# Optimization experiments

Hardware: AMD Instinct MI355X
Metric: run time of the kernel (lower is better)

Reference implementation:

```python
import jax, jax.numpy as jnp
import numpy as np

EPS = 1e-06        # normalize eps and log eps (module's self.eps)
PDIST_EPS = 1e-06  # torch.nn.PairwiseDistance default eps: ||x1 - x2 + eps||_2

A, C, F = 4096, 8, 64


def setup_inputs() -> dict:
    key = jax.random.key(0)
    x = jax.random.normal(key, (A, C, F), dtype=jnp.float32)
    return {"x": x}


def reference(x) -> jnp.ndarray:
    a = x.shape[0]
    c = x.shape[1]
    # F.normalize(p=2, dim=-1, eps=EPS): x / max(||x||_2, eps)
    nrm = jnp.linalg.norm(x, axis=-1, keepdims=True)
    xn = x / jnp.maximum(nrm, EPS)
    # pairwise cosine similarity per group: [C, A, A]
    sim = jnp.einsum('acf,bcf->cab', xn, xn)
    # mask self-similarity on the diagonal with -1
    diag = jnp.eye(a, dtype=bool)[None, :, :]
    sim = jnp.where(diag, -1.0, sim)
    # nearest neighbor per (c, a): argmax over b -> [C, A] -> [A, C]
    idx = jnp.argmax(sim, axis=-1).T
    # gather matched embeddings: x_match[a, c, f] = xn[idx[a, c], c, f]
    x_match = xn[idx, jnp.arange(c)[None, :], :]
    # PairwiseDistance(p=2, eps=1e-6): ||x - x_match + eps||_2 over last dim
    min_dist = jnp.linalg.norm(xn - x_match + PDIST_EPS, axis=-1)
    loss = -jnp.mean(jnp.log(min_dist + EPS))
    return loss
```

## Files before the change

### kernel.cpp

```cpp
#include <hip/hip_runtime.h>
#include <math.h>

#define AN 4096
#define CN 8
#define FN 64
#define ACN (AN*CN)

typedef __attribute__((ext_vector_type(8))) short bf16x8;
typedef __attribute__((ext_vector_type(4))) float f32x4;

__device__ inline unsigned short f2bf(float f) {
    unsigned u = __float_as_uint(f);
    unsigned r = ((u >> 16) & 1) + 0x7FFFu;
    return (unsigned short)((u + r) >> 16);
}

__global__ __launch_bounds__(256) void k1_normalize(const float* __restrict__ x,
                                                    unsigned short* __restrict__ xnb,
                                                    float* __restrict__ inv)
{
    int tid  = threadIdx.x;
    int grp  = tid >> 4;
    int slot = tid & 15;
    #pragma unroll
    for (int s = 0; s < 4; ++s) {
        int V = blockIdx.x * 64 + s * 16 + grp;
        const float4 v = *(const float4*)(x + (size_t)V * FN + slot * 4);
        float ss = v.x*v.x + v.y*v.y + v.z*v.z + v.w*v.w;
        ss += __shfl_xor(ss, 1);
        ss += __shfl_xor(ss, 2);
        ss += __shfl_xor(ss, 4);
        ss += __shfl_xor(ss, 8);
        float sc = 1.0f / fmaxf(sqrtf(ss), 1e-6f);
        int a = V >> 3, c = V & 7;
        ushort4 ob;
        ob.x = f2bf(v.x * sc); ob.y = f2bf(v.y * sc);
        ob.z = f2bf(v.z * sc); ob.w = f2bf(v.w * sc);
        *(ushort4*)(xnb + ((size_t)c * AN + a) * FN + slot * 4) = ob;
        if (slot == 0) inv[V] = sc;
    }
}

__global__ __launch_bounds__(256, 2) void k2_argmax(const unsigned short* __restrict__ xnb,
                                                    unsigned int* __restrict__ pP)
{
    __shared__ uint4 lds4[3 * 1024];

    int blk  = blockIdx.x;
    int half = blk & 1;
    int rt   = (blk >> 1) & 31;
    int c    = blk >> 6;
    int a0   = rt * 128;
    int b0base = half * 2048;

    const uint4* __restrict__ Xc4 = (const uint4*)(xnb + (size_t)c * AN * FN);

    int tid  = threadIdx.x;
    int lane = tid & 63;
    int w    = tid >> 6;
    int wr   = w >> 1;
    int wc   = w & 1;
    int l15  = lane & 15;
    int quad = lane >> 4;

    int srow   = tid >> 3;
    int schunk = tid & 7;

    #pragma unroll
    for (int s = 0; s < 4; ++s) {
        int r = srow + 32 * s;
        lds4[r * 8 + (schunk ^ (r & 7))] = Xc4[(size_t)(a0 + r) * 8 + schunk];
    }
    #pragma unroll
    for (int s = 0; s < 4; ++s) {
        int r = srow + 32 * s;
        lds4[1024 + r * 8 + (schunk ^ (r & 7))] = Xc4[(size_t)(b0base + r) * 8 + schunk];
    }
    __syncthreads();

    bf16x8 afr[4][2];
    #pragma unroll
    for (int mi = 0; mi < 4; ++mi)
        #pragma unroll
        for (int ks = 0; ks < 2; ++ks) {
            int r  = wr * 64 + mi * 16 + l15;
            int ch = (ks * 4 + quad) ^ (r & 7);
            afr[mi][ks] = ((const bf16x8*)lds4)[r * 8 + ch];
        }

    float bestp[16];
    #pragma unroll
    for (int i = 0; i < 16; ++i) bestp[i] = 0.0f;

    const f32x4 two = {2.0f, 2.0f, 2.0f, 2.0f};

    for (int it = 0; it < 16; ++it) {
        int cur = it & 1;
        uint4 gv[4];
        if (it < 15) {
            int g0 = b0base + (it + 1) * 128;
            #pragma unroll
            for (int s = 0; s < 4; ++s)
                gv[s] = Xc4[(size_t)(g0 + srow + 32 * s) * 8 + schunk];
        }

        f32x4 acc[4][4];
        const bf16x8* bt = (const bf16x8*)(lds4 + 1024 + cur * 1024);
        #pragma unroll
        for (int ks = 0; ks < 2; ++ks) {
            #pragma unroll
            for (int ni = 0; ni < 4; ++ni) {
                int r  = wc * 64 + ni * 16 + l15;
                int ch = (ks * 4 + quad) ^ (r & 7);
                bf16x8 bfr = bt[r * 8 + ch];
                #pragma unroll
                for (int mi = 0; mi < 4; ++mi)
                    acc[mi][ni] = __builtin_amdgcn_mfma_f32_16x16x32_bf16(
                        afr[mi][ks], bfr, (ks == 0) ? two : acc[mi][ni], 0, 0, 0);
            }
        }

        int colblk = b0base + it * 128 + wc * 64;
        int codebase = colblk + l15;
        #pragma unroll
        for (int mi = 0; mi < 4; ++mi) {
            int rfrag = a0 + wr * 64 + mi * 16;
            #pragma unroll
            for (int r = 0; r < 4; ++r) {
                float cand[4];
                #pragma unroll
                for (int ni = 0; ni < 4; ++ni) {
                    unsigned pb = (__float_as_uint(acc[mi][ni][r]) & 0xFFFFF000u)
                                | (unsigned)(codebase + ni * 16);
                    cand[ni] = __uint_as_float(pb);
                }
                #pragma unroll
                for (int ni = 0; ni < 4; ++ni) {
                    if (rfrag == colblk + ni * 16) {
                        if (l15 == quad * 4 + r) cand[ni] = 0.0f;
                    }
                }
                int bi = mi * 4 + r;
                bestp[bi] = fmaxf(fmaxf(fmaxf(fmaxf(cand[0], cand[1]), cand[2]),
                                        cand[3]), bestp[bi]);
            }
        }

        if (it < 15) {
            #pragma unroll
            for (int s = 0; s < 4; ++s) {
                int r = srow + 32 * s;
                lds4[1024 + (cur ^ 1) * 1024 + r * 8 + (schunk ^ (r & 7))] = gv[s];
            }
        }
        __syncthreads();
    }

    #pragma unroll
    for (int i = 0; i < 16; ++i) {
        float v = bestp[i];
        v = fmaxf(v, __shfl_xor(v, 1));
        v = fmaxf(v, __shfl_xor(v, 2));
        v = fmaxf(v, __shfl_xor(v, 4));
        v = fmaxf(v, __shfl_xor(v, 8));
        bestp[i] = v;
    }
    __syncthreads();
    float* red = (float*)lds4;
    if (l15 == 0) {
        #pragma unroll
        for (int mi = 0; mi < 4; ++mi)
            #pragma unroll
            for (int r = 0; r < 4; ++r)
                red[w * 64 + mi * 16 + quad * 4 + r] = bestp[mi * 4 + r];
    }
    __syncthreads();
    if (tid < 128) {
        int wr2 = tid >> 6, r64 = tid & 63;
        float p = fmaxf(red[(2 * wr2) * 64 + r64], red[(2 * wr2 + 1) * 64 + r64]);
        int a = a0 + tid;
        pP[(size_t)half * ACN + (size_t)a * CN + c] = __float_as_uint(p);
    }
}

__global__ __launch_bounds__(256) void k3_dist(const float* __restrict__ x,
                                               const float* __restrict__ inv,
                                               const unsigned int* __restrict__ pP,
                                               float* __restrict__ partials)
{
    int tid = threadIdx.x;
    int id = blockIdx.x * 256 + tid;
    float p0 = __uint_as_float(pP[id]);
    float p1 = __uint_as_float(pP[ACN + id]);
    unsigned pm = __float_as_uint(fmaxf(p0, p1));
    int m = (int)(pm & 0xFFFu);
    int c = id & 7;
    int idb = m * CN + c;
    float sa = inv[id];
    float sb = inv[idb];
    const float* xa = x + (size_t)id  * FN;
    const float* xb = x + (size_t)idb * FN;
    float ss = 0.0f;
    #pragma unroll
    for (int q = 0; q < 16; ++q) {
        float4 va = *(const float4*)(xa + 4 * q);
        float4 vb = *(const float4*)(xb + 4 * q);
        float d0 = va.x * sa - vb.x * sb + 1e-6f;
        float d1 = va.y * sa - vb.y * sb + 1e-6f;
        float d2 = va.z * sa - vb.z * sb + 1e-6f;
        float d3 = va.w * sa - vb.w * sb + 1e-6f;
        ss += d0*d0 + d1*d1 + d2*d2 + d3*d3;
    }
    float val = logf(sqrtf(ss) + 1e-6f);

    float t = val;
    #pragma unroll
    for (int off = 32; off > 0; off >>= 1) t += __shfl_down(t, off);
    __shared__ float ws4[4];
    if ((tid & 63) == 0) ws4[tid >> 6] = t;
    __syncthreads();
    if (tid == 0)
        partials[blockIdx.x] = ws4[0] + ws4[1] + ws4[2] + ws4[3];
}

__global__ __launch_bounds__(64) void k4_final(const float* __restrict__ partials,
                                               float* __restrict__ out)
{
    int t = threadIdx.x;
    float v = partials[t] + partials[t + 64];
    #pragma unroll
    for (int off = 32; off > 0; off >>= 1) v += __shfl_down(v, off);
    if (t == 0) out[0] = -v / (float)ACN;
}

extern "C" void kernel_launch(void* const* d_in, const int* in_sizes, int n_in,
                              void* d_out, int out_size, void* d_ws, size_t ws_size,
                              hipStream_t stream)
{
    const float* x = (const float*)d_in[0];
    unsigned short* xnb = (unsigned short*)d_ws;
    float* inv = (float*)(xnb + (size_t)AN * CN * FN);
    unsigned int* pP = (unsigned int*)(inv + ACN);
    float* partials = (float*)(pP + 2 * ACN);

    k1_normalize<<<512, 256, 0, stream>>>(x, xnb, inv);
    k2_argmax  <<<512, 256, 0, stream>>>(xnb, pP);
    k3_dist    <<<128, 256, 0, stream>>>(x, inv, pP, partials);
    k4_final   <<<1, 64, 0, stream>>>(partials, (float*)d_out);
}
```

Baseline: 91.92 us.

## Use direct global-to-LDS loads and remap warps to full-row column strips

Replaces register-staged global loads plus LDS stores with global_load_lds direct copies into LDS, keeping the XOR swizzle by permuting the global source chunk. Each wave now holds all 128 A rows (8 fragments) and handles a 32-column strip of each B tile instead of a 64x64 quadrant, which changes the per-wave MFMA tiling and the epilogue reduction. The intent is to cut VGPR staging and LDS write instructions and to overlap the prefetch better. In exchange, A-fragment and best-value register usage doubles, which may pressure occupancy under launch_bounds(256,2).

```diff
diff --git a/kernel.cpp b/kernel.cpp
--- a/kernel.cpp
+++ b/kernel.cpp
@@ -8,6 +8,11 @@
 
 typedef __attribute__((ext_vector_type(8))) short bf16x8;
 typedef __attribute__((ext_vector_type(4))) float f32x4;
+
+#define GLL16(gsrc, ldst) \
+    __builtin_amdgcn_global_load_lds( \
+        (const __attribute__((address_space(1))) void*)(gsrc), \
+        (__attribute__((address_space(3))) void*)(ldst), 16, 0, 0)
 
 __device__ inline unsigned short f2bf(float f) {
     unsigned u = __float_as_uint(f);
@@ -53,111 +58,103 @@
     int a0   = rt * 128;
     int b0base = half * 2048;
 
-    const uint4* __restrict__ Xc4 = (const uint4*)(xnb + (size_t)c * AN * FN);
+    const char* __restrict__ Xc = (const char*)(xnb + (size_t)c * AN * FN);
 
     int tid  = threadIdx.x;
     int lane = tid & 63;
     int w    = tid >> 6;
-    int wr   = w >> 1;
-    int wc   = w & 1;
     int l15  = lane & 15;
     int quad = lane >> 4;
 
-    int srow   = tid >> 3;
-    int schunk = tid & 7;
+    int srow  = lane >> 3;
+    int sslot = lane & 7;
 
     #pragma unroll
     for (int s = 0; s < 4; ++s) {
-        int r = srow + 32 * s;
-        lds4[r * 8 + (schunk ^ (r & 7))] = Xc4[(size_t)(a0 + r) * 8 + schunk];
-    }
-    #pragma unroll
-    for (int s = 0; s < 4; ++s) {
-        int r = srow + 32 * s;
-        lds4[1024 + r * 8 + (schunk ^ (r & 7))] = Xc4[(size_t)(b0base + r) * 8 + schunk];
-    }
-    __syncthreads();
-
-    bf16x8 afr[4][2];
-    #pragma unroll
-    for (int mi = 0; mi < 4; ++mi)
+        int base = (w * 4 + s) * 64;
+        int row  = (base >> 3) + srow;
+        int gch  = sslot ^ (row & 7);
+        size_t gb = (size_t)row * 128 + (size_t)gch * 16;
+        GLL16(Xc + (size_t)(a0) * 128 + gb,      lds4 + base);
+        GLL16(Xc + (size_t)(b0base) * 128 + gb,  lds4 + 1024 + base);
+    }
+    __syncthreads();
+
+    bf16x8 afr[8][2];
+    #pragma unroll
+    for (int mi = 0; mi < 8; ++mi)
         #pragma unroll
         for (int ks = 0; ks < 2; ++ks) {
-            int r  = wr * 64 + mi * 16 + l15;
+            int r  = mi * 16 + l15;
             int ch = (ks * 4 + quad) ^ (r & 7);
             afr[mi][ks] = ((const bf16x8*)lds4)[r * 8 + ch];
         }
 
-    float bestp[16];
-    #pragma unroll
-    for (int i = 0; i < 16; ++i) bestp[i] = 0.0f;
+    float bestp[32];
+    #pragma unroll
+    for (int i = 0; i < 32; ++i) bestp[i] = 0.0f;
 
     const f32x4 two = {2.0f, 2.0f, 2.0f, 2.0f};
 
     for (int it = 0; it < 16; ++it) {
         int cur = it & 1;
-        uint4 gv[4];
+
         if (it < 15) {
             int g0 = b0base + (it + 1) * 128;
             #pragma unroll
-            for (int s = 0; s < 4; ++s)
-                gv[s] = Xc4[(size_t)(g0 + srow + 32 * s) * 8 + schunk];
-        }
-
-        f32x4 acc[4][4];
+            for (int s = 0; s < 4; ++s) {
+                int base = (w * 4 + s) * 64;
+                int row  = (base >> 3) + srow;
+                int gch  = sslot ^ (row & 7);
+                GLL16(Xc + (size_t)(g0 + row) * 128 + (size_t)gch * 16,
+                      lds4 + 1024 + (cur ^ 1) * 1024 + base);
+            }
+        }
+
+        f32x4 acc[8][2];
         const bf16x8* bt = (const bf16x8*)(lds4 + 1024 + cur * 1024);
         #pragma unroll
         for (int ks = 0; ks < 2; ++ks) {
             #pragma unroll
-            for (int ni = 0; ni < 4; ++ni) {
-                int r  = wc * 64 + ni * 16 + l15;
+            for (int ni = 0; ni < 2; ++ni) {
+                int r  = w * 32 + ni * 16 + l15;
                 int ch = (ks * 4 + quad) ^ (r & 7);
                 bf16x8 bfr = bt[r * 8 + ch];
                 #pragma unroll
-                for (int mi = 0; mi < 4; ++mi)
+                for (int mi = 0; mi < 8; ++mi)
                     acc[mi][ni] = __builtin_amdgcn_mfma_f32_16x16x32_bf16(
                         afr[mi][ks], bfr, (ks == 0) ? two : acc[mi][ni], 0, 0, 0);
             }
         }
 
-        int colblk = b0base + it * 128 + wc * 64;
-        int codebase = colblk + l15;
-        #pragma unroll
-        for (int mi = 0; mi < 4; ++mi) {
-            int rfrag = a0 + wr * 64 + mi * 16;
+        int colblk = b0base + it * 128 + w * 32;
+        #pragma unroll
+        for (int mi = 0; mi < 8; ++mi) {
+            int rfrag = a0 + mi * 16;
             #pragma unroll
             for (int r = 0; r < 4; ++r) {
-                float cand[4];
-                #pragma unroll
-                for (int ni = 0; ni < 4; ++ni) {
-                    unsigned pb = (__float_as_uint(acc[mi][ni][r]) & 0xFFFFF000u)
-                                | (unsigned)(codebase + ni * 16);
-                    cand[ni] = __uint_as_float(pb);
+                unsigned p0 = (__float_as_uint(acc[mi][0][r]) & 0xFFFFF000u)
+                            | (unsigned)(colblk + l15);
+                unsigned p1 = (__float_as_uint(acc[mi][1][r]) & 0xFFFFF000u)
+                            | (unsigned)(colblk + 16 + l15);
+                float c0 = __uint_as_float(p0);
+                float c1 = __uint_as_float(p1);
+                if (rfrag == colblk) {
+                    if (l15 == quad * 4 + r) c0 = 0.0f;
                 }
-                #pragma unroll
-                for (int ni = 0; ni < 4; ++ni) {
-                    if (rfrag == colblk + ni * 16) {
-                        if (l15 == quad * 4 + r) cand[ni] = 0.0f;
-                    }
+                if (rfrag == colblk + 16) {
+                    if (l15 == quad * 4 + r) c1 = 0.0f;
                 }
                 int bi = mi * 4 + r;
-                bestp[bi] = fmaxf(fmaxf(fmaxf(fmaxf(cand[0], cand[1]), cand[2]),
-                                        cand[3]), bestp[bi]);
+                bestp[bi] = fmaxf(fmaxf(c0, c1), bestp[bi]);
             }
         }
 
-        if (it < 15) {
-            #pragma unroll
-            for (int s = 0; s < 4; ++s) {
-                int r = srow + 32 * s;
-                lds4[1024 + (cur ^ 1) * 1024 + r * 8 + (schunk ^ (r & 7))] = gv[s];
-            }
-        }
         __syncthreads();
     }
 
     #pragma unroll
-    for (int i = 0; i < 16; ++i) {
+    for (int i = 0; i < 32; ++i) {
         float v = bestp[i];
         v = fmaxf(v, __shfl_xor(v, 1));
         v = fmaxf(v, __shfl_xor(v, 2));
@@ -169,15 +166,15 @@
     float* red = (float*)lds4;
     if (l15 == 0) {
         #pragma unroll
-        for (int mi = 0; mi < 4; ++mi)
+        for (int mi = 0; mi < 8; ++mi)
             #pragma unroll
             for (int r = 0; r < 4; ++r)
-                red[w * 64 + mi * 16 + quad * 4 + r] = bestp[mi * 4 + r];
+                red[w * 128 + mi * 16 + quad * 4 + r] = bestp[mi * 4 + r];
     }
     __syncthreads();
     if (tid < 128) {
-        int wr2 = tid >> 6, r64 = tid & 63;
-        float p = fmaxf(red[(2 * wr2) * 64 + r64], red[(2 * wr2 + 1) * 64 + r64]);
+        float p = fmaxf(fmaxf(red[tid], red[128 + tid]),
+                        fmaxf(red[256 + tid], red[384 + tid]));
         int a = a0 + tid;
         pP[(size_t)half * ACN + (size_t)a * CN + c] = __float_as_uint(p);
     }
```

Measured after the change: 94.56 us. 1.03x slower.
